# Kernel optimization log

Measured on AMD Instinct MI355X. Metric: run time of the kernel, lower is better.

Reference implementation:

```python
import jax, jax.numpy as jnp
import numpy as np
import math

BOUND = 1e-06
PI = math.pi

N_DIMS = 256
N_ROWS = 524288
DELTA = 1e-06


def _make_buffers(n_dims, delta, radius, scaling, range_type="bound"):
    if range_type == "whole":
        phi_L = 0.0
    else:  # 'bound'
        L = 0.01
        upper_bound = PI / 2 * (1.0 - L)
        phi_L = math.asin(delta ** (1.0 / n_dims))
        phi_L = phi_L if phi_L < upper_bound else upper_bound
    # W_theta: identity with last row duplicated -> (n_dims+1, n_dims)
    eye = np.eye(n_dims, dtype=np.float32)
    W_theta = np.concatenate([eye, eye[-1:]], axis=0)
    # W_phi: strictly upper-triangular ones, with [-2, -1] zeroed
    W_phi = np.triu(np.ones((n_dims + 1, n_dims + 1), dtype=np.float32), k=1)
    W_phi[-2, -1] = 0.0
    b_phi = np.zeros(n_dims + 1, dtype=np.float32)
    b_phi[-1] = -PI / 2.0
    return (
        jnp.float32(phi_L),
        jnp.asarray(W_theta),
        jnp.asarray(W_phi),
        jnp.asarray(b_phi),
        jnp.float32(radius),
        jnp.float32(scaling),
    )


def setup_inputs() -> dict:
    key = jax.random.key(0)
    x = jax.random.normal(key, (N_ROWS, N_DIMS), dtype=jnp.float32)
    phi_L, W_theta, W_phi, b_phi, radius, scaling = _make_buffers(
        N_DIMS, DELTA, radius=1.0, scaling=1.0, range_type="bound"
    )
    return {
        "x": x,
        "W_theta": W_theta,
        "W_phi": W_phi,
        "b_phi": b_phi,
        "phi_L": phi_L,
        "radius": radius,
        "scaling": scaling,
    }


def reference(x, W_theta, W_phi, b_phi, phi_L, radius, scaling):
    # Map features to angles in [phi_L, pi/2)
    ang = (PI / 2 - phi_L) * jax.nn.sigmoid(scaling * x) + phi_L
    # Duplicate last angle: [N, n_dims] -> [N, n_dims+1]
    a = jnp.matmul(ang, W_theta.T)
    # log-sin cumulative sum (via strictly-upper-triangular matmul) + log-cos term
    logx = jnp.matmul(jnp.log(jnp.sin(a) + BOUND), W_phi) + jnp.log(
        jnp.cos(a + b_phi) + BOUND
    )
    return radius * jnp.exp(logx)
```

## Files before the change

kernel.cpp:

```cpp
#include <hip/hip_runtime.h>

#define BOUND 1e-6f
#define HALF_PI 1.57079632679489662f
#define LOG2E 1.44269504088896341f

#define UPD_DPP(oldv, srcv, ctrl, rmask)                                        \
  __int_as_float(__builtin_amdgcn_update_dpp(                                   \
      __float_as_int(oldv), __float_as_int(srcv), (ctrl), (rmask), 0xF, false))

__device__ __forceinline__ float wave_incl_prod(float x) {
    x *= UPD_DPP(1.0f, x, 0x111, 0xF);
    x *= UPD_DPP(1.0f, x, 0x112, 0xF);
    x *= UPD_DPP(1.0f, x, 0x114, 0xF);
    x *= UPD_DPP(1.0f, x, 0x118, 0xF);
    x *= UPD_DPP(1.0f, x, 0x142, 0xA);
    x *= UPD_DPP(1.0f, x, 0x143, 0xC);
    return x;
}

__global__ __launch_bounds__(256) void spherize_kernel(
    const float* __restrict__ x,
    const float* __restrict__ p_phiL,
    const float* __restrict__ p_radius,
    const float* __restrict__ p_scaling,
    float* __restrict__ out,
    int n_rows)
{
    __shared__ float lds[16 * 257];

    const float phi_L   = p_phiL[0];
    const float radius  = p_radius[0];
    const float cexp    = p_scaling[0] * LOG2E;
    const float amp     = HALF_PI - phi_L;

    const int tid  = threadIdx.x;
    const int lane = tid & 63;
    const int wave = tid >> 6;
    const int row0 = blockIdx.x * 16;
    const int wrow = row0 + wave * 4;

    const int nr_blk = min(16, n_rows - row0);
    const int nr_w   = min(4, max(0, n_rows - wrow));

    float4 xv[4];
    const float* xb = x + (size_t)wrow * 256 + lane * 4;
    #pragma unroll
    for (int i = 0; i < 4; ++i)
        if (i < nr_w) xv[i] = *reinterpret_cast<const float4*>(xb + i * 256);

    #pragma unroll
    for (int i = 0; i < 4; ++i) {
        if (i >= nr_w) break;
        const float* xp = &xv[i].x;
        float s[4], c[4];
        #pragma unroll
        for (int k = 0; k < 4; ++k) {
            float e  = __builtin_amdgcn_exp2f(cexp * xp[k]);
            float u  = amp * __builtin_amdgcn_rcpf(1.0f + e);
            float u2 = u * u;
            s[k] = fmaf(u2, fmaf(u2, 4.16666667e-2f, -0.5f), 1.0f + BOUND);
            float p = fmaf(u2, fmaf(u2, 8.33333333e-3f, -1.66666667e-1f), 1.0f);
            c[k] = fmaf(u, p, BOUND);
        }

        float q1 = s[0];
        float q2 = q1 * s[1];
        float q3 = q2 * s[2];
        float t  = q3 * s[3];
        float scan = wave_incl_prod(t);
        float excl = UPD_DPP(1.0f, scan, 0x138, 0xF);
        float base = radius * excl;

        float* lrow = lds + (wave * 4 + i) * 257 + lane * 4;
        lrow[0] = base * c[0];
        lrow[1] = base * q1 * c[1];
        lrow[2] = base * q2 * c[2];
        lrow[3] = base * q3 * c[3];
        if (lane == 63)
            lrow[4] = radius * scan;
    }
    __syncthreads();

    float* obase = out + (size_t)row0 * 257;
    if (nr_blk == 16) {
        const float4* l4 = reinterpret_cast<const float4*>(lds);
        float4*       o4 = reinterpret_cast<float4*>(obase);
        o4[tid]        = l4[tid];
        o4[tid + 256]  = l4[tid + 256];
        o4[tid + 512]  = l4[tid + 512];
        o4[tid + 768]  = l4[tid + 768];
        if (tid < 4) o4[tid + 1024] = l4[tid + 1024];
    } else {
        const int nd = nr_blk * 257;
        for (int i = tid; i < nd; i += 256) obase[i] = lds[i];
    }
}

extern "C" void kernel_launch(void* const* d_in, const int* in_sizes, int n_in,
                              void* d_out, int out_size, void* d_ws, size_t ws_size,
                              hipStream_t stream) {
    const float* x         = (const float*)d_in[0];
    const float* p_phiL    = (const float*)d_in[4];
    const float* p_radius  = (const float*)d_in[5];
    const float* p_scaling = (const float*)d_in[6];
    float* out = (float*)d_out;

    const int n_rows = in_sizes[0] / 256;
    const int blocks = (n_rows + 15) / 16;

    spherize_kernel<<<blocks, 256, 0, stream>>>(x, p_phiL, p_radius, p_scaling,
                                                out, n_rows);
}
```

Measured before the change: 204.1 us.

## Make kernel persistent with register prefetch and double-buffered LDS staging

Launches a fixed grid of up to 1024 blocks that walk 16-row chunks in grid-stride order, instead of one block per chunk. Each block prefetches the next chunk's input into registers while it computes and stores the current one. LDS is double-buffered so a single barrier per chunk is enough. The aim is to overlap global loads with compute and stores and to cut block launch overhead, at the cost of fewer resident waves per CU from the doubled LDS and the fixed grid size.

```diff
diff --git a/kernel.cpp b/kernel.cpp
--- a/kernel.cpp
+++ b/kernel.cpp
@@ -24,75 +24,99 @@
     const float* __restrict__ p_radius,
     const float* __restrict__ p_scaling,
     float* __restrict__ out,
-    int n_rows)
+    int n_rows, int nchunks)
 {
-    __shared__ float lds[16 * 257];
+    __shared__ float lds[2][16 * 257];
 
     const float phi_L   = p_phiL[0];
     const float radius  = p_radius[0];
     const float cexp    = p_scaling[0] * LOG2E;
     const float amp     = HALF_PI - phi_L;
 
-    const int tid  = threadIdx.x;
-    const int lane = tid & 63;
-    const int wave = tid >> 6;
-    const int row0 = blockIdx.x * 16;
-    const int wrow = row0 + wave * 4;
+    const int tid    = threadIdx.x;
+    const int lane   = tid & 63;
+    const int wave   = tid >> 6;
+    const int stride = gridDim.x;
 
-    const int nr_blk = min(16, n_rows - row0);
-    const int nr_w   = min(4, max(0, n_rows - wrow));
+    auto LOADC = [&](float4 (&r)[4], int c) {
+        const int wrow = c * 16 + wave * 4;
+        const float* xb = x + (size_t)wrow * 256 + lane * 4;
+        #pragma unroll
+        for (int i = 0; i < 4; ++i)
+            if (wrow + i < n_rows)
+                r[i] = *reinterpret_cast<const float4*>(xb + i * 256);
+    };
 
-    float4 xv[4];
-    const float* xb = x + (size_t)wrow * 256 + lane * 4;
-    #pragma unroll
-    for (int i = 0; i < 4; ++i)
-        if (i < nr_w) xv[i] = *reinterpret_cast<const float4*>(xb + i * 256);
+    auto COMPUTE = [&](float4 (&r)[4], int c, float* buf) {
+        const int wrow = c * 16 + wave * 4;
+        #pragma unroll
+        for (int i = 0; i < 4; ++i) {
+            if (wrow + i >= n_rows) break;
+            const float* xp = &r[i].x;
+            float s[4], cc[4];
+            #pragma unroll
+            for (int k = 0; k < 4; ++k) {
+                float e  = __builtin_amdgcn_exp2f(cexp * xp[k]);
+                float u  = amp * __builtin_amdgcn_rcpf(1.0f + e);
+                float u2 = u * u;
+                s[k] = fmaf(u2, fmaf(u2, 4.16666667e-2f, -0.5f), 1.0f + BOUND);
+                float p = fmaf(u2, fmaf(u2, 8.33333333e-3f, -1.66666667e-1f), 1.0f);
+                cc[k] = fmaf(u, p, BOUND);
+            }
+            float q1 = s[0];
+            float q2 = q1 * s[1];
+            float q3 = q2 * s[2];
+            float t  = q3 * s[3];
+            float scan = wave_incl_prod(t);
+            float excl = UPD_DPP(1.0f, scan, 0x138, 0xF);
+            float base = radius * excl;
 
-    #pragma unroll
-    for (int i = 0; i < 4; ++i) {
-        if (i >= nr_w) break;
-        const float* xp = &xv[i].x;
-        float s[4], c[4];
-        #pragma unroll
-        for (int k = 0; k < 4; ++k) {
-            float e  = __builtin_amdgcn_exp2f(cexp * xp[k]);
-            float u  = amp * __builtin_amdgcn_rcpf(1.0f + e);
-            float u2 = u * u;
-            s[k] = fmaf(u2, fmaf(u2, 4.16666667e-2f, -0.5f), 1.0f + BOUND);
-            float p = fmaf(u2, fmaf(u2, 8.33333333e-3f, -1.66666667e-1f), 1.0f);
-            c[k] = fmaf(u, p, BOUND);
+            float* lrow = buf + (wave * 4 + i) * 257 + lane * 4;
+            lrow[0] = base * cc[0];
+            lrow[1] = base * q1 * cc[1];
+            lrow[2] = base * q2 * cc[2];
+            lrow[3] = base * q3 * cc[3];
+            if (lane == 63)
+                lrow[4] = radius * scan;
         }
+        asm volatile("s_waitcnt lgkmcnt(0)\n\ts_barrier" ::: "memory");
+    };
 
-        float q1 = s[0];
-        float q2 = q1 * s[1];
-        float q3 = q2 * s[2];
-        float t  = q3 * s[3];
-        float scan = wave_incl_prod(t);
-        float excl = UPD_DPP(1.0f, scan, 0x138, 0xF);
-        float base = radius * excl;
+    auto STOREC = [&](int c, const float* buf) {
+        const int row0 = c * 16;
+        float* obase = out + (size_t)row0 * 257;
+        const int nrb = min(16, n_rows - row0);
+        if (nrb == 16) {
+            const float4* l4 = reinterpret_cast<const float4*>(buf);
+            float4*       o4 = reinterpret_cast<float4*>(obase);
+            o4[tid]       = l4[tid];
+            o4[tid + 256] = l4[tid + 256];
+            o4[tid + 512] = l4[tid + 512];
+            o4[tid + 768] = l4[tid + 768];
+            if (tid < 4) o4[tid + 1024] = l4[tid + 1024];
+        } else {
+            const int nd = nrb * 257;
+            for (int i = tid; i < nd; i += 256) obase[i] = buf[i];
+        }
+    };
 
-        float* lrow = lds + (wave * 4 + i) * 257 + lane * 4;
-        lrow[0] = base * c[0];
-        lrow[1] = base * q1 * c[1];
-        lrow[2] = base * q2 * c[2];
-        lrow[3] = base * q3 * c[3];
-        if (lane == 63)
-            lrow[4] = radius * scan;
-    }
-    __syncthreads();
+    int c = blockIdx.x;
+    if (c >= nchunks) return;
 
-    float* obase = out + (size_t)row0 * 257;
-    if (nr_blk == 16) {
-        const float4* l4 = reinterpret_cast<const float4*>(lds);
-        float4*       o4 = reinterpret_cast<float4*>(obase);
-        o4[tid]        = l4[tid];
-        o4[tid + 256]  = l4[tid + 256];
-        o4[tid + 512]  = l4[tid + 512];
-        o4[tid + 768]  = l4[tid + 768];
-        if (tid < 4) o4[tid + 1024] = l4[tid + 1024];
-    } else {
-        const int nd = nr_blk * 257;
-        for (int i = tid; i < nd; i += 256) obase[i] = lds[i];
+    float4 xA[4], xB[4];
+    LOADC(xA, c);
+    for (;;) {
+        const int c1 = c + stride;
+        if (c1 < nchunks) LOADC(xB, c1);
+        COMPUTE(xA, c, lds[0]);
+        STOREC(c, lds[0]);
+        if (c1 >= nchunks) break;
+        const int c2 = c1 + stride;
+        if (c2 < nchunks) LOADC(xA, c2);
+        COMPUTE(xB, c1, lds[1]);
+        STOREC(c1, lds[1]);
+        if (c2 >= nchunks) break;
+        c = c2;
     }
 }
 
@@ -105,9 +129,11 @@
     const float* p_scaling = (const float*)d_in[6];
     float* out = (float*)d_out;
 
-    const int n_rows = in_sizes[0] / 256;
-    const int blocks = (n_rows + 15) / 16;
+    const int n_rows  = in_sizes[0] / 256;
+    const int nchunks = (n_rows + 15) / 16;
+    int blocks = 1024;
+    if (blocks > nchunks) blocks = nchunks;
 
     spherize_kernel<<<blocks, 256, 0, stream>>>(x, p_phiL, p_radius, p_scaling,
-                                                out, n_rows);
+                                                out, n_rows, nchunks);
 }
```

Result: slower. 219.0 us (+7.3%).

## Persistent per-wave grid-stride loop with double-buffered row-group prefetch

Applied to the files above, without the earlier changes.

Replaces the one-block-per-16-rows launch with a fixed grid of 2048 blocks. Each wave independently loops over 4-row groups with a stride. Loads for the next group are issued into a second register buffer before the current group is processed, so global reads overlap with compute and stores. Each wave now stages rows in its own LDS slice and waits only on its own LDS traffic instead of a block-wide barrier. The risks are higher register pressure from the double buffer and less parallelism in flight than a full oversubscribed grid for this memory-bound kernel.

```diff
diff --git a/kernel.cpp b/kernel.cpp
--- a/kernel.cpp
+++ b/kernel.cpp
@@ -24,75 +24,93 @@
     const float* __restrict__ p_radius,
     const float* __restrict__ p_scaling,
     float* __restrict__ out,
-    int n_rows)
+    int n_rows, int n_groups, int total_waves)
 {
-    __shared__ float lds[16 * 257];
+    __shared__ float lds[4 * 1028];
 
-    const float phi_L   = p_phiL[0];
-    const float radius  = p_radius[0];
-    const float cexp    = p_scaling[0] * LOG2E;
-    const float amp     = HALF_PI - phi_L;
+    const float phi_L  = p_phiL[0];
+    const float radius = p_radius[0];
+    const float cexp   = p_scaling[0] * LOG2E;
+    const float amp    = HALF_PI - phi_L;
 
-    const int tid  = threadIdx.x;
-    const int lane = tid & 63;
-    const int wave = tid >> 6;
-    const int row0 = blockIdx.x * 16;
-    const int wrow = row0 + wave * 4;
+    const int lane = threadIdx.x & 63;
+    const int wave = threadIdx.x >> 6;
+    float* myl = lds + wave * 1028;
 
-    const int nr_blk = min(16, n_rows - row0);
-    const int nr_w   = min(4, max(0, n_rows - wrow));
+    auto LOADG = [&](float4 (&r)[4], int g) {
+        const int r0 = g * 4;
+        const float* xb = x + (size_t)r0 * 256 + lane * 4;
+        #pragma unroll
+        for (int i = 0; i < 4; ++i)
+            if (r0 + i < n_rows)
+                r[i] = *reinterpret_cast<const float4*>(xb + i * 256);
+    };
 
-    float4 xv[4];
-    const float* xb = x + (size_t)wrow * 256 + lane * 4;
-    #pragma unroll
-    for (int i = 0; i < 4; ++i)
-        if (i < nr_w) xv[i] = *reinterpret_cast<const float4*>(xb + i * 256);
+    auto PROC = [&](const float4 (&r)[4], int g) {
+        const int r0 = g * 4;
+        const int nr = min(4, n_rows - r0);
+        #pragma unroll
+        for (int i = 0; i < 4; ++i) {
+            if (i >= nr) break;
+            const float* xp = &r[i].x;
+            float s[4], cc[4];
+            #pragma unroll
+            for (int k = 0; k < 4; ++k) {
+                float e  = __builtin_amdgcn_exp2f(cexp * xp[k]);
+                float u  = amp * __builtin_amdgcn_rcpf(1.0f + e);
+                float u2 = u * u;
+                s[k] = fmaf(u2, fmaf(u2, 4.16666667e-2f, -0.5f), 1.0f + BOUND);
+                float p = fmaf(u2, fmaf(u2, 8.33333333e-3f, -1.66666667e-1f), 1.0f);
+                cc[k] = fmaf(u, p, BOUND);
+            }
+            float q1 = s[0];
+            float q2 = q1 * s[1];
+            float q3 = q2 * s[2];
+            float t  = q3 * s[3];
+            float scan = wave_incl_prod(t);
+            float excl = UPD_DPP(1.0f, scan, 0x138, 0xF);
+            float base = radius * excl;
 
-    #pragma unroll
-    for (int i = 0; i < 4; ++i) {
-        if (i >= nr_w) break;
-        const float* xp = &xv[i].x;
-        float s[4], c[4];
-        #pragma unroll
-        for (int k = 0; k < 4; ++k) {
-            float e  = __builtin_amdgcn_exp2f(cexp * xp[k]);
-            float u  = amp * __builtin_amdgcn_rcpf(1.0f + e);
-            float u2 = u * u;
-            s[k] = fmaf(u2, fmaf(u2, 4.16666667e-2f, -0.5f), 1.0f + BOUND);
-            float p = fmaf(u2, fmaf(u2, 8.33333333e-3f, -1.66666667e-1f), 1.0f);
-            c[k] = fmaf(u, p, BOUND);
+            float* lrow = myl + i * 257 + lane * 4;
+            lrow[0] = base * cc[0];
+            lrow[1] = base * q1 * cc[1];
+            lrow[2] = base * q2 * cc[2];
+            lrow[3] = base * q3 * cc[3];
+            if (lane == 63)
+                lrow[4] = radius * scan;
         }
+        asm volatile("s_waitcnt lgkmcnt(0)" ::: "memory");
 
-        float q1 = s[0];
-        float q2 = q1 * s[1];
-        float q3 = q2 * s[2];
-        float t  = q3 * s[3];
-        float scan = wave_incl_prod(t);
-        float excl = UPD_DPP(1.0f, scan, 0x138, 0xF);
-        float base = radius * excl;
+        float* obase = out + (size_t)r0 * 257;
+        if (nr == 4) {
+            const float4* l4 = reinterpret_cast<const float4*>(myl);
+            float4*       o4 = reinterpret_cast<float4*>(obase);
+            o4[lane]       = l4[lane];
+            o4[lane + 64]  = l4[lane + 64];
+            o4[lane + 128] = l4[lane + 128];
+            o4[lane + 192] = l4[lane + 192];
+            if (lane == 0) o4[256] = l4[256];
+        } else {
+            const int nd = nr * 257;
+            for (int j = lane; j < nd; j += 64) obase[j] = myl[j];
+        }
+    };
 
-        float* lrow = lds + (wave * 4 + i) * 257 + lane * 4;
-        lrow[0] = base * c[0];
-        lrow[1] = base * q1 * c[1];
-        lrow[2] = base * q2 * c[2];
-        lrow[3] = base * q3 * c[3];
-        if (lane == 63)
-            lrow[4] = radius * scan;
-    }
-    __syncthreads();
+    int g = blockIdx.x * 4 + wave;
+    if (g >= n_groups) return;
 
-    float* obase = out + (size_t)row0 * 257;
-    if (nr_blk == 16) {
-        const float4* l4 = reinterpret_cast<const float4*>(lds);
-        float4*       o4 = reinterpret_cast<float4*>(obase);
-        o4[tid]        = l4[tid];
-        o4[tid + 256]  = l4[tid + 256];
-        o4[tid + 512]  = l4[tid + 512];
-        o4[tid + 768]  = l4[tid + 768];
-        if (tid < 4) o4[tid + 1024] = l4[tid + 1024];
-    } else {
-        const int nd = nr_blk * 257;
-        for (int i = tid; i < nd; i += 256) obase[i] = lds[i];
+    float4 A[4], B[4];
+    LOADG(A, g);
+    for (;;) {
+        const int g1 = g + total_waves;
+        if (g1 < n_groups) LOADG(B, g1);
+        PROC(A, g);
+        if (g1 >= n_groups) break;
+        const int g2 = g1 + total_waves;
+        if (g2 < n_groups) LOADG(A, g2);
+        PROC(B, g1);
+        if (g2 >= n_groups) break;
+        g = g2;
     }
 }
 
@@ -105,9 +123,12 @@
     const float* p_scaling = (const float*)d_in[6];
     float* out = (float*)d_out;
 
-    const int n_rows = in_sizes[0] / 256;
-    const int blocks = (n_rows + 15) / 16;
+    const int n_rows   = in_sizes[0] / 256;
+    const int n_groups = (n_rows + 3) / 4;
+    int blocks = 2048;
+    if (blocks * 4 > n_groups) blocks = (n_groups + 3) / 4;
+    const int total_waves = blocks * 4;
 
     spherize_kernel<<<blocks, 256, 0, stream>>>(x, p_phiL, p_radius, p_scaling,
-                                                out, n_rows);
+                                                out, n_rows, n_groups, total_waves);
 }
```

Measured after the change: 216.4 us. 1.06x slower.
